# Optimization experiments

Measured on AMD Instinct MI355X. Metric: run time of the kernel, lower is better.

## Reference

```python
import jax, jax.numpy as jnp
import numpy as np

B, L, H, E = 2, 2048, 16, 64  # S == L (causal self-attention), D == E


def setup_inputs() -> dict:
    key = jax.random.key(0)
    kq, kk, kv, ks = jax.random.split(key, 4)
    queries = jax.random.normal(kq, (B, L, H, E), dtype=jnp.float32)
    keys = jax.random.normal(kk, (B, L, H, E), dtype=jnp.float32)
    values = jax.random.normal(kv, (B, L, H, E), dtype=jnp.float32)
    # TriangularCausalMask: True above the diagonal -> masked out
    attn_mask = jnp.broadcast_to(
        jnp.triu(jnp.ones((L, L), dtype=bool), k=1)[None, None], (B, 1, L, L)
    )
    init_score = jax.random.uniform(ks, (B, L, L), dtype=jnp.float32)
    return {
        "queries": queries,
        "keys": keys,
        "values": values,
        "attn_mask": attn_mask,
        "init_score": init_score,
    }


def reference(queries, keys, values, attn_mask, init_score):
    # queries: [B,L,H,E], keys: [B,S,H,E], values: [B,S,H,D]
    E_ = queries.shape[-1]
    scale = 1.0 / np.sqrt(E_).astype(np.float32)
    # scores: [B,H,L,S]
    scores = jnp.einsum('blhe,bshe->bhls', queries, keys)
    scores = jnp.where(attn_mask, -jnp.inf, scores)
    A = jax.nn.softmax(scale * scores, axis=-1)  # dropout p=0 -> identity
    # post-softmax bias, broadcast over heads
    A = A + 0.1 * init_score[:, None, :, :]
    # V: [B,L,H,D]
    V = jnp.einsum('bhls,bshd->blhd', A, values)
    return V
```

## Files before the change

kernel.cpp:

```cpp
#include <hip/hip_runtime.h>
#include <hip/hip_bf16.h>
#include <math.h>

#define BB 2
#define LL 2048
#define HH 16
#define EE 64
#define LOG2E 1.44269504089f

typedef __attribute__((ext_vector_type(8))) short short8;
typedef __attribute__((ext_vector_type(4))) float floatx4;
typedef unsigned int u32;

union S8 { short8 v; u32 u[4]; ushort4 q[2]; };

__device__ inline u32 pkbf(float lo, float hi) {
    union { __hip_bfloat162 h; u32 u; } c;
    c.h = __float22bfloat162_rn(make_float2(lo, hi));
    return c.u;
}

__device__ inline ushort4 cvt4(float4 v) {
    union { __hip_bfloat162 h; u32 u; } a, b;
    a.h = __float22bfloat162_rn(make_float2(v.x, v.y));
    b.h = __float22bfloat162_rn(make_float2(v.z, v.w));
    ushort4 r;
    r.x = (unsigned short)(a.u & 0xffffu);
    r.y = (unsigned short)(a.u >> 16);
    r.z = (unsigned short)(b.u & 0xffffu);
    r.w = (unsigned short)(b.u >> 16);
    return r;
}

__device__ inline short8 pack8(float4 a, float4 b) {
    S8 s; s.q[0] = cvt4(a); s.q[1] = cvt4(b); return s.v;
}

__device__ inline void async16(unsigned short* lds, const unsigned short* g) {
    __builtin_amdgcn_global_load_lds(
        (const __attribute__((address_space(1))) u32*)g,
        (__attribute__((address_space(3))) u32*)lds, 16, 0, 0);
}

__global__ __launch_bounds__(256) void prepass(
    const float* __restrict__ k, const float* __restrict__ v,
    const float* __restrict__ isc, unsigned short* __restrict__ kb,
    unsigned short* __restrict__ vt, unsigned short* __restrict__ isb)
{
    const int bid = blockIdx.x;
    const int t = threadIdx.x;
    if (bid < 1024) {
        #pragma unroll
        for (int it = 0; it < 2; ++it) {
            int idx = bid * 512 + it * 256 + t;
            const float4* src = (const float4*)k + idx * 2;
            float4 a = src[0], c = src[1];
            int e8 = idx & 7, h = (idx >> 3) & 15, l = (idx >> 7) & 2047, b = idx >> 18;
            *(short8*)&kb[(((b * 16 + h) * 2048 + l) * 64) + e8 * 8] = pack8(a, c);
        }
    } else if (bid < 2048) {
        const int ib = bid - 1024;
        #pragma unroll
        for (int it = 0; it < 4; ++it) {
            int idx = ib * 1024 + it * 256 + t;
            const float4* src = (const float4*)isc + idx * 2;
            float4 a = src[0], c = src[1];
            a.x *= 0.1f; a.y *= 0.1f; a.z *= 0.1f; a.w *= 0.1f;
            c.x *= 0.1f; c.y *= 0.1f; c.z *= 0.1f; c.w *= 0.1f;
            ((short8*)isb)[idx] = pack8(a, c);
        }
    } else {
        __shared__ float Tf[64][68];
        const int vb = bid - 2048;
        const int st = vb & 31, h = (vb >> 5) & 15, b = vb >> 9;
        const int s0 = st * 64;
        #pragma unroll
        for (int i = 0; i < 4; ++i) {
            int r = i * 16 + (t >> 4), c = (t & 15) * 4;
            float4 val = *(const float4*)(v + (((b * LL + s0 + r) * HH + h) * EE) + c);
            *(float4*)&Tf[r][c] = val;
        }
        __syncthreads();
        #pragma unroll
        for (int i = 0; i < 4; ++i) {
            int d = i * 16 + (t >> 4), s4 = (t & 15) * 4;
            float4 val = make_float4(Tf[s4 + 0][d], Tf[s4 + 1][d],
                                     Tf[s4 + 2][d], Tf[s4 + 3][d]);
            *(ushort4*)&vt[((b * 16 + h) * 64 + d) * 2048 + s0 + s4] = cvt4(val);
        }
    }
}

template <int MODE>
__device__ __forceinline__ void tile_step(
    const unsigned short* __restrict__ Ks, const unsigned short* __restrict__ Vs,
    const short8 qf[2], const short8 isf[2],
    floatx4 o_attn[4], floatx4 o_bias[4], float& lsum,
    int s0, int mbase, int wave, int lq, int ln, int lnl,
    int alo, int ahi, bool hisel)
{
    u32 pk[4][2];
    if (MODE < 2) {
        #pragma unroll
        for (int sb = 0; sb < 4; ++sb) {
            if (MODE == 1 && wave < sb) { pk[sb][0] = 0; pk[sb][1] = 0; continue; }
            short8 kf0 = *(const short8*)&Ks[(sb * 16 + ln) * 64 + ((lq ^ lnl) << 3)];
            short8 kf1 = *(const short8*)&Ks[(sb * 16 + ln) * 64 + (((4 + lq) ^ lnl) << 3)];
            floatx4 sa = {0.f, 0.f, 0.f, 0.f};
            sa = __builtin_amdgcn_mfma_f32_16x16x32_bf16(kf0, qf[0], sa, 0, 0, 0);
            sa = __builtin_amdgcn_mfma_f32_16x16x32_bf16(kf1, qf[1], sa, 0, 0, 0);
            float pv[4];
            #pragma unroll
            for (int r = 0; r < 4; ++r) {
                float t = sa[r];
                if (MODE == 1 && (s0 + sb * 16 + lq * 4 + r) > (mbase + ln)) t = -INFINITY;
                float p = exp2f(t);
                lsum += p;
                pv[r] = p;
            }
            pk[sb][0] = pkbf(pv[0], pv[1]);
            pk[sb][1] = pkbf(pv[2], pv[3]);
        }
    }
    #pragma unroll
    for (int kk = 0; kk < 2; ++kk) {
        short8 vf[4];
        #pragma unroll
        for (int db = 0; db < 4; ++db)
            vf[db] = *(const short8*)&Vs[(db * 16 + ln) * 64 + (((kk * 4 + lq) ^ lnl) << 3)];
        short8 af = isf[kk];
        #pragma unroll
        for (int db = 0; db < 4; ++db)
            o_bias[db] = __builtin_amdgcn_mfma_f32_16x16x32_bf16(af, vf[db], o_bias[db], 0, 0, 0);
        if (MODE < 2) {
            S8 pf;
            u32 a0 = (u32)__builtin_amdgcn_ds_bpermute(alo, (int)pk[kk * 2][0]);
            u32 b0 = (u32)__builtin_amdgcn_ds_bpermute(alo, (int)pk[kk * 2 + 1][0]);
            pf.u[0] = hisel ? b0 : a0;
            u32 a1 = (u32)__builtin_amdgcn_ds_bpermute(alo, (int)pk[kk * 2][1]);
            u32 b1 = (u32)__builtin_amdgcn_ds_bpermute(alo, (int)pk[kk * 2 + 1][1]);
            pf.u[1] = hisel ? b1 : a1;
            u32 a2 = (u32)__builtin_amdgcn_ds_bpermute(ahi, (int)pk[kk * 2][0]);
            u32 b2 = (u32)__builtin_amdgcn_ds_bpermute(ahi, (int)pk[kk * 2 + 1][0]);
            pf.u[2] = hisel ? b2 : a2;
            u32 a3 = (u32)__builtin_amdgcn_ds_bpermute(ahi, (int)pk[kk * 2][1]);
            u32 b3 = (u32)__builtin_amdgcn_ds_bpermute(ahi, (int)pk[kk * 2 + 1][1]);
            pf.u[3] = hisel ? b3 : a3;
            #pragma unroll
            for (int db = 0; db < 4; ++db)
                o_attn[db] = __builtin_amdgcn_mfma_f32_16x16x32_bf16(pf.v, vf[db], o_attn[db], 0, 0, 0);
        }
    }
}

__global__ __launch_bounds__(256, 4) void fused6(
    const float* __restrict__ q, const unsigned short* __restrict__ kb,
    const unsigned short* __restrict__ vt, const unsigned short* __restrict__ isb,
    float* __restrict__ out)
{
    __shared__ unsigned short Ks[2][64 * 64];
    __shared__ unsigned short Vs[2][64 * 64];

    const int tid = threadIdx.x, lane = tid & 63, wave = tid >> 6;
    const int lq = lane >> 4, ln = lane & 15, lnl = ln & 7;

    const int bid = blockIdx.x;
    const int h = bid & 15, b = (bid >> 4) & 1, g = bid >> 5;
    int qt;
    if (g < 8) qt = 31 - g;
    else if (g < 16) qt = g;
    else if (g < 24) qt = 39 - g;
    else qt = g - 24;
    const int q0 = qt * 64;
    const int mbase = q0 + wave * 16;

    short8 qf[2];
    {
        const float sc = 0.125f * LOG2E;
        const float* qrow = q + (((long)(b * LL + mbase + ln)) * HH + h) * EE;
        #pragma unroll
        for (int kk = 0; kk < 2; ++kk) {
            float4 a = *(const float4*)(qrow + kk * 32 + lq * 8);
            float4 c = *(const float4*)(qrow + kk * 32 + lq * 8 + 4);
            a.x *= sc; a.y *= sc; a.z *= sc; a.w *= sc;
            c.x *= sc; c.y *= sc; c.z *= sc; c.w *= sc;
            qf[kk] = pack8(a, c);
        }
    }

    const unsigned short* kbh = kb + (long)(b * HH + h) * (LL * EE);
    const unsigned short* vth = vt + (long)(b * HH + h) * (EE * LL);

    floatx4 o_attn[4], o_bias[4];
    #pragma unroll
    for (int db = 0; db < 4; ++db) {
        o_attn[db] = (floatx4){0.f, 0.f, 0.f, 0.f};
        o_bias[db] = (floatx4){0.f, 0.f, 0.f, 0.f};
    }
    float lsum = 0.f;

    const int rr = lane >> 3, jl = lane & 7;
    const int swz = (jl ^ rr) * 8;
    const unsigned short* ksrc0 = kbh + (wave * 16 + rr) * 64 + swz;
    const unsigned short* ksrc1 = kbh + (wave * 16 + 8 + rr) * 64 + swz;
    const unsigned short* vsrc0 = vth + (wave * 16 + rr) * LL + swz;
    const unsigned short* vsrc1 = vth + (wave * 16 + 8 + rr) * LL + swz;

    const unsigned short* isrow =
        isb + (long)(b * LL + q0 + wave * 16 + ln) * LL + lq * 8;

    const int alo = (((lq & 1) * 2) * 16 + ln) * 4;
    const int ahi = (((lq & 1) * 2 + 1) * 16 + ln) * 4;
    const bool hisel = (lq >= 2);

    auto issue = [&](int j) {
        const int s0 = j * 64, bsel = j & 1;
        if (j <= qt) {
            async16(&Ks[bsel][(wave * 16) * 64], ksrc0 + s0 * 64);
            async16(&Ks[bsel][(wave * 16 + 8) * 64], ksrc1 + s0 * 64);
        }
        async16(&Vs[bsel][(wave * 16) * 64], vsrc0 + s0);
        async16(&Vs[bsel][(wave * 16 + 8) * 64], vsrc1 + s0);
    };

    short8 isf[2], isfn[2];
    auto ldnext = [&](int j, short8* dst) {
        int jc = j < 32 ? j : 31;
        dst[0] = *(const short8*)(isrow + jc * 64);
        dst[1] = *(const short8*)(isrow + jc * 64 + 32);
    };

    ldnext(0, isf);
    issue(0);
    for (int j = 0; j < qt; ++j) {
        __syncthreads();
        issue(j + 1);
        ldnext(j + 1, isfn);
        tile_step<0>(Ks[j & 1], Vs[j & 1], qf, isf, o_attn, o_bias, lsum,
                     j * 64, mbase, wave, lq, ln, lnl, alo, ahi, hisel);
        isf[0] = isfn[0]; isf[1] = isfn[1];
    }
    {
        __syncthreads();
        if (qt < 31) issue(qt + 1);
        ldnext(qt + 1, isfn);
        tile_step<1>(Ks[qt & 1], Vs[qt & 1], qf, isf, o_attn, o_bias, lsum,
                     q0, mbase, wave, lq, ln, lnl, alo, ahi, hisel);
        isf[0] = isfn[0]; isf[1] = isfn[1];
    }
    for (int j = qt + 1; j < 32; ++j) {
        __syncthreads();
        if (j < 31) issue(j + 1);
        ldnext(j + 1, isfn);
        tile_step<2>(Vs[j & 1], Vs[j & 1], qf, isf, o_attn, o_bias, lsum,
                     j * 64, mbase, wave, lq, ln, lnl, alo, ahi, hisel);
        isf[0] = isfn[0]; isf[1] = isfn[1];
    }

    float s = lsum;
    s += __shfl_xor(s, 16);
    s += __shfl_xor(s, 32);
    #pragma unroll
    for (int r = 0; r < 4; ++r) {
        float inv = 1.0f / __shfl(s, lq * 4 + r);
        int m = mbase + lq * 4 + r;
        float* ob = out + (((long)(b * LL + m)) * HH + h) * EE;
        #pragma unroll
        for (int db = 0; db < 4; ++db)
            ob[db * 16 + ln] = o_attn[db][r] * inv + o_bias[db][r];
    }
}

extern "C" void kernel_launch(void* const* d_in, const int* in_sizes, int n_in,
                              void* d_out, int out_size, void* d_ws, size_t ws_size,
                              hipStream_t stream) {
    (void)in_sizes; (void)n_in; (void)out_size; (void)ws_size;
    const float* q   = (const float*)d_in[0];
    const float* k   = (const float*)d_in[1];
    const float* v   = (const float*)d_in[2];
    const float* isc = (const float*)d_in[4];
    float* out = (float*)d_out;

    unsigned short* kb  = (unsigned short*)d_ws;
    unsigned short* vt  = (unsigned short*)((char*)d_ws + (8u << 20));
    unsigned short* isb = (unsigned short*)((char*)d_ws + (16u << 20));

    prepass<<<dim3(3072), dim3(256), 0, stream>>>(k, v, isc, kb, vt, isb);
    fused6<<<dim3(1024), dim3(256), 0, stream>>>(q, kb, vt, isb, out);
}
```

Baseline: 197.9 us.

## Compute softmax row sums via MFMA with ones, add setprio, rework V transpose

The softmax denominator is now accumulated with an extra MFMA of the bf16 probabilities against a ones vector, replacing per-lane scalar adds and the final shuffles. This also makes the denominator use the same bf16-rounded probabilities as the numerator. MFMA groups are wrapped in s_setprio to raise wave priority during matrix work. In the prepass, the V-transpose blocks are reordered ahead of the bias blocks, use a 69-column padded LDS tile, and write 8-element bf16 stores instead of 4-element ones.

```diff
diff --git a/kernel.cpp b/kernel.cpp
--- a/kernel.cpp
+++ b/kernel.cpp
@@ -59,7 +59,29 @@
             *(short8*)&kb[(((b * 16 + h) * 2048 + l) * 64) + e8 * 8] = pack8(a, c);
         }
     } else if (bid < 2048) {
-        const int ib = bid - 1024;
+        __shared__ float Tf[64][69];
+        const int vb = bid - 1024;
+        const int st = vb & 31, h = (vb >> 5) & 15, b = vb >> 9;
+        const int s0 = st * 64;
+        #pragma unroll
+        for (int i = 0; i < 4; ++i) {
+            int r = i * 16 + (t >> 4), c = (t & 15) * 4;
+            float4 val = *(const float4*)(v + (((b * LL + s0 + r) * HH + h) * EE) + c);
+            *(float4*)&Tf[r][c] = val;
+        }
+        __syncthreads();
+        #pragma unroll
+        for (int i = 0; i < 2; ++i) {
+            int slot = t + i * 256;
+            int d = slot >> 3, s8 = (slot & 7) * 8;
+            float4 lo = make_float4(Tf[s8 + 0][d], Tf[s8 + 1][d],
+                                    Tf[s8 + 2][d], Tf[s8 + 3][d]);
+            float4 hi = make_float4(Tf[s8 + 4][d], Tf[s8 + 5][d],
+                                    Tf[s8 + 6][d], Tf[s8 + 7][d]);
+            *(short8*)&vt[((b * 16 + h) * 64 + d) * 2048 + s0 + s8] = pack8(lo, hi);
+        }
+    } else {
+        const int ib = bid - 2048;
         #pragma unroll
         for (int it = 0; it < 4; ++it) {
             int idx = ib * 1024 + it * 256 + t;
@@ -69,33 +91,14 @@
             c.x *= 0.1f; c.y *= 0.1f; c.z *= 0.1f; c.w *= 0.1f;
             ((short8*)isb)[idx] = pack8(a, c);
         }
-    } else {
-        __shared__ float Tf[64][68];
-        const int vb = bid - 2048;
-        const int st = vb & 31, h = (vb >> 5) & 15, b = vb >> 9;
-        const int s0 = st * 64;
-        #pragma unroll
-        for (int i = 0; i < 4; ++i) {
-            int r = i * 16 + (t >> 4), c = (t & 15) * 4;
-            float4 val = *(const float4*)(v + (((b * LL + s0 + r) * HH + h) * EE) + c);
-            *(float4*)&Tf[r][c] = val;
-        }
-        __syncthreads();
-        #pragma unroll
-        for (int i = 0; i < 4; ++i) {
-            int d = i * 16 + (t >> 4), s4 = (t & 15) * 4;
-            float4 val = make_float4(Tf[s4 + 0][d], Tf[s4 + 1][d],
-                                     Tf[s4 + 2][d], Tf[s4 + 3][d]);
-            *(ushort4*)&vt[((b * 16 + h) * 64 + d) * 2048 + s0 + s4] = cvt4(val);
-        }
     }
 }
 
 template <int MODE>
 __device__ __forceinline__ void tile_step(
     const unsigned short* __restrict__ Ks, const unsigned short* __restrict__ Vs,
-    const short8 qf[2], const short8 isf[2],
-    floatx4 o_attn[4], floatx4 o_bias[4], float& lsum,
+    const short8 qf[2], const short8 isf[2], const short8 ones,
+    floatx4 o_attn[4], floatx4 o_bias[4], floatx4& o_sum,
     int s0, int mbase, int wave, int lq, int ln, int lnl,
     int alo, int ahi, bool hisel)
 {
@@ -107,16 +110,16 @@
             short8 kf0 = *(const short8*)&Ks[(sb * 16 + ln) * 64 + ((lq ^ lnl) << 3)];
             short8 kf1 = *(const short8*)&Ks[(sb * 16 + ln) * 64 + (((4 + lq) ^ lnl) << 3)];
             floatx4 sa = {0.f, 0.f, 0.f, 0.f};
+            __builtin_amdgcn_s_setprio(1);
             sa = __builtin_amdgcn_mfma_f32_16x16x32_bf16(kf0, qf[0], sa, 0, 0, 0);
             sa = __builtin_amdgcn_mfma_f32_16x16x32_bf16(kf1, qf[1], sa, 0, 0, 0);
+            __builtin_amdgcn_s_setprio(0);
             float pv[4];
             #pragma unroll
             for (int r = 0; r < 4; ++r) {
                 float t = sa[r];
                 if (MODE == 1 && (s0 + sb * 16 + lq * 4 + r) > (mbase + ln)) t = -INFINITY;
-                float p = exp2f(t);
-                lsum += p;
-                pv[r] = p;
+                pv[r] = exp2f(t);
             }
             pk[sb][0] = pkbf(pv[0], pv[1]);
             pk[sb][1] = pkbf(pv[2], pv[3]);
@@ -129,9 +132,11 @@
         for (int db = 0; db < 4; ++db)
             vf[db] = *(const short8*)&Vs[(db * 16 + ln) * 64 + (((kk * 4 + lq) ^ lnl) << 3)];
         short8 af = isf[kk];
+        __builtin_amdgcn_s_setprio(1);
         #pragma unroll
         for (int db = 0; db < 4; ++db)
             o_bias[db] = __builtin_amdgcn_mfma_f32_16x16x32_bf16(af, vf[db], o_bias[db], 0, 0, 0);
+        __builtin_amdgcn_s_setprio(0);
         if (MODE < 2) {
             S8 pf;
             u32 a0 = (u32)__builtin_amdgcn_ds_bpermute(alo, (int)pk[kk * 2][0]);
@@ -146,14 +151,17 @@
             u32 a3 = (u32)__builtin_amdgcn_ds_bpermute(ahi, (int)pk[kk * 2][1]);
             u32 b3 = (u32)__builtin_amdgcn_ds_bpermute(ahi, (int)pk[kk * 2 + 1][1]);
             pf.u[3] = hisel ? b3 : a3;
+            __builtin_amdgcn_s_setprio(1);
+            o_sum = __builtin_amdgcn_mfma_f32_16x16x32_bf16(pf.v, ones, o_sum, 0, 0, 0);
             #pragma unroll
             for (int db = 0; db < 4; ++db)
                 o_attn[db] = __builtin_amdgcn_mfma_f32_16x16x32_bf16(pf.v, vf[db], o_attn[db], 0, 0, 0);
-        }
-    }
-}
-
-__global__ __launch_bounds__(256, 4) void fused6(
+            __builtin_amdgcn_s_setprio(0);
+        }
+    }
+}
+
+__global__ __launch_bounds__(256, 4) void fused10(
     const float* __restrict__ q, const unsigned short* __restrict__ kb,
     const unsigned short* __restrict__ vt, const unsigned short* __restrict__ isb,
     float* __restrict__ out)
@@ -197,7 +205,9 @@
         o_attn[db] = (floatx4){0.f, 0.f, 0.f, 0.f};
         o_bias[db] = (floatx4){0.f, 0.f, 0.f, 0.f};
     }
-    float lsum = 0.f;
+    floatx4 o_sum = (floatx4){0.f, 0.f, 0.f, 0.f};
+    const short8 ones = {(short)0x3F80, (short)0x3F80, (short)0x3F80, (short)0x3F80,
+                         (short)0x3F80, (short)0x3F80, (short)0x3F80, (short)0x3F80};
 
     const int rr = lane >> 3, jl = lane & 7;
     const int swz = (jl ^ rr) * 8;
@@ -236,7 +246,7 @@
         __syncthreads();
         issue(j + 1);
         ldnext(j + 1, isfn);
-        tile_step<0>(Ks[j & 1], Vs[j & 1], qf, isf, o_attn, o_bias, lsum,
+        tile_step<0>(Ks[j & 1], Vs[j & 1], qf, isf, ones, o_attn, o_bias, o_sum,
                      j * 64, mbase, wave, lq, ln, lnl, alo, ahi, hisel);
         isf[0] = isfn[0]; isf[1] = isfn[1];
     }
@@ -244,7 +254,7 @@
         __syncthreads();
         if (qt < 31) issue(qt + 1);
         ldnext(qt + 1, isfn);
-        tile_step<1>(Ks[qt & 1], Vs[qt & 1], qf, isf, o_attn, o_bias, lsum,
+        tile_step<1>(Ks[qt & 1], Vs[qt & 1], qf, isf, ones, o_attn, o_bias, o_sum,
                      q0, mbase, wave, lq, ln, lnl, alo, ahi, hisel);
         isf[0] = isfn[0]; isf[1] = isfn[1];
     }
@@ -252,17 +262,14 @@
         __syncthreads();
         if (j < 31) issue(j + 1);
         ldnext(j + 1, isfn);
-        tile_step<2>(Vs[j & 1], Vs[j & 1], qf, isf, o_attn, o_bias, lsum,
+        tile_step<2>(Vs[j & 1], Vs[j & 1], qf, isf, ones, o_attn, o_bias, o_sum,
                      j * 64, mbase, wave, lq, ln, lnl, alo, ahi, hisel);
         isf[0] = isfn[0]; isf[1] = isfn[1];
     }
 
-    float s = lsum;
-    s += __shfl_xor(s, 16);
-    s += __shfl_xor(s, 32);
     #pragma unroll
     for (int r = 0; r < 4; ++r) {
-        float inv = 1.0f / __shfl(s, lq * 4 + r);
+        float inv = 1.0f / o_sum[r];
         int m = mbase + lq * 4 + r;
         float* ob = out + (((long)(b * LL + m)) * HH + h) * EE;
         #pragma unroll
@@ -286,5 +293,5 @@
     unsigned short* isb = (unsigned short*)((char*)d_ws + (16u << 20));
 
     prepass<<<dim3(3072), dim3(256), 0, stream>>>(k, v, isc, kb, vt, isb);
-    fused6<<<dim3(1024), dim3(256), 0, stream>>>(q, kb, vt, isb, out);
-}
+    fused10<<<dim3(1024), dim3(256), 0, stream>>>(q, kb, vt, isb, out);
+}
```

After: 196.4 us. No clear change (-0.8%).
